# Optimization experiments

Measured on AMD Instinct MI355X. Metric: run time of the kernel, lower is better.

The kernel has to match this reference:

```python
import jax, jax.numpy as jnp
import numpy as np

N_USERS = 100000
N_ITEMS = 50000
N_NODES = N_USERS + N_ITEMS
D = 64
N_INTENTS = 128
N_LAYERS = 2
E = 3200000
E_U = 1600000
E_I = 800000
N_MP = 2


def spmm(idx, vals, x, n):
    # sparse (n,n) COO @ dense (n,d): out[r] = sum_e vals[e] * x[c[e]] where idx=[rows;cols]
    return jax.ops.segment_sum(vals[:, None] * x[idx[1]], idx[0], num_segments=n)


def graph_conv_both(edges, h, n):
    # DGL GraphConv(norm='both', weight=None, bias=None, allow_zero_in_degree=True)
    src, dst = edges[0], edges[1]
    ones = jnp.ones(src.shape[0], h.dtype)
    deg_out = jax.ops.segment_sum(ones, src, num_segments=n)
    deg_in = jax.ops.segment_sum(ones, dst, num_segments=n)
    inv = lambda d: jnp.where(d > 0, jax.lax.rsqrt(jnp.maximum(d, 1e-12)), 0.0)
    hs = h * inv(deg_out)[:, None]
    agg = jax.ops.segment_sum(hs[src], dst, num_segments=n)
    return agg * inv(deg_in)[:, None]


def semantic_attention(z, W1, b1, w2):
    # z: (N, M, D)
    w = jnp.tanh(z @ W1 + b1) @ w2        # (N, M)
    beta = jax.nn.softmax(w.mean(0))       # (M,)
    return jnp.einsum('m,nmd->nd', beta, z)


def dccf(G_indices, G_values, feat_user, feat_item, user_intent, item_intent):
    emb = jnp.concatenate([feat_user, feat_item], axis=0)
    total = emb
    cur = emb
    for _ in range(N_LAYERS):
        gnn = spmm(G_indices, G_values, cur, N_NODES)
        u, it = cur[:N_USERS], cur[N_USERS:]
        u_int = jax.nn.softmax(u @ user_intent, axis=1) @ user_intent.T
        i_int = jax.nn.softmax(it @ item_intent, axis=1) @ item_intent.T
        cur = gnn + jnp.concatenate([u_int, i_int], axis=0) + cur
        total = total + cur
    return total[:N_USERS], total[N_USERS:]


def han(mp_edges, h, n, W1, b1, w2):
    z = jnp.stack([graph_conv_both(mp_edges[m], h, n) for m in range(N_MP)], axis=1)
    return semantic_attention(z, W1, b1, w2)


def setup_inputs() -> dict:
    key = jax.random.key(0)
    ks = jax.random.split(key, 16)
    s = 1.0 / np.sqrt(D)
    return {
        'G_indices': jax.random.randint(ks[0], (2, E), 0, N_NODES),
        'G_values': jax.random.uniform(ks[1], (E,), jnp.float32),
        'feat_user': jax.random.normal(ks[2], (N_USERS, D), jnp.float32) * s,
        'feat_item': jax.random.normal(ks[3], (N_ITEMS, D), jnp.float32) * s,
        'user_intent': jax.random.normal(ks[4], (D, N_INTENTS), jnp.float32) * s,
        'item_intent': jax.random.normal(ks[5], (D, N_INTENTS), jnp.float32) * s,
        'mp_user_edges': jax.random.randint(ks[6], (N_MP, 2, E_U), 0, N_USERS),
        'mp_item_edges': jax.random.randint(ks[7], (N_MP, 2, E_I), 0, N_ITEMS),
        'sem_user_W1': jax.random.normal(ks[8], (D, 128), jnp.float32) * s,
        'sem_user_b1': jnp.zeros((128,), jnp.float32),
        'sem_user_w2': jax.random.normal(ks[9], (128,), jnp.float32) * s,
        'sem_item_W1': jax.random.normal(ks[10], (D, 128), jnp.float32) * s,
        'sem_item_b1': jnp.zeros((128,), jnp.float32),
        'sem_item_w2': jax.random.normal(ks[11], (128,), jnp.float32) * s,
        'user_idx': jax.random.randint(ks[12], (1024,), 0, N_USERS),
        'item_idx': jax.random.randint(ks[13], (1024,), 0, N_ITEMS),
        'neg_item_idx': jax.random.randint(ks[14], (1024,), 0, N_ITEMS),
    }


def reference(G_indices, G_values, feat_user, feat_item, user_intent, item_intent,
              mp_user_edges, mp_item_edges,
              sem_user_W1, sem_user_b1, sem_user_w2,
              sem_item_W1, sem_item_b1, sem_item_w2,
              user_idx, item_idx, neg_item_idx):
    ua, ia = dccf(G_indices, G_values, feat_user, feat_item, user_intent, item_intent)
    h_user = han(mp_user_edges, feat_user, N_USERS, sem_user_W1, sem_user_b1, sem_user_w2)
    h_item = han(mp_item_edges, feat_item, N_ITEMS, sem_item_W1, sem_item_b1, sem_item_w2)
    user_emb = 0.5 * ua + 0.5 * h_user
    item_emb = 0.5 * ia + 0.5 * h_item
    return (user_emb, item_emb)
```

## Files before the change

### kernel.cpp

```cpp
#include <hip/hip_runtime.h>
#include <hip/hip_bf16.h>
#include <math.h>

#define N_USERS 100000
#define N_ITEMS 50000
#define N_NODES 150000
#define DD 64
#define E_G 3200000
#define EU 1600000
#define EI 800000
#define E_HAN 4800000
#define NH 300000
#define NBG 293
#define NBH 586
#define ROWS 32

__device__ __forceinline__ float invdeg(float d){
  return d > 0.f ? rsqrtf(fmaxf(d, 1e-12f)) : 0.f;
}
__device__ __forceinline__ float tanh_fast(float x){
  float cx = fminf(15.f, fmaxf(-15.f, x));
  float t = __expf(2.f*cx);
  return (t - 1.f)/(t + 1.f);
}
__device__ __forceinline__ unsigned short f2b(float x){
  unsigned int b = __float_as_uint(x);
  b += 0x7FFFu + ((b >> 16) & 1u);
  return (unsigned short)(b >> 16);
}
__device__ __forceinline__ float b2f(unsigned short u){
  return __uint_as_float(((unsigned int)u) << 16);
}
__device__ __forceinline__ float b2f_lo(unsigned int u){
  return __uint_as_float(u << 16);
}
__device__ __forceinline__ float b2f_hi(unsigned int u){
  return __uint_as_float(u & 0xFFFF0000u);
}

__global__ void k_init(const float* __restrict__ fu, const float* __restrict__ fi,
                       float* __restrict__ cur, float* __restrict__ total){
  int i = blockIdx.x*256 + threadIdx.x;
  if (i >= N_NODES*DD) return;
  float v = (i < N_USERS*DD) ? fu[i] : fi[i - N_USERS*DD];
  cur[i] = v; total[i] = v;
}

__global__ __launch_bounds__(256) void k_colscan(int* __restrict__ wh, int nb,
                                                 int* __restrict__ colsum){
  __shared__ int s[256];
  int b = blockIdx.x, tid = threadIdx.x;
  int v = wh[tid*nb + b];
  s[tid] = v; __syncthreads();
  for (int o = 1; o < 256; o <<= 1){
    int t = (tid >= o) ? s[tid - o] : 0;
    __syncthreads();
    s[tid] += t;
    __syncthreads();
  }
  wh[tid*nb + b] = s[tid] - v;
  if (tid == 255) colsum[b] = s[255];
}

__global__ __launch_bounds__(256) void k_bscan(const int* __restrict__ colsum, int nb,
                                               int total, int* __restrict__ bB){
  __shared__ int s[256];
  __shared__ int carry;
  int tid = threadIdx.x;
  if (tid == 0) carry = 0;
  __syncthreads();
  for (int base = 0; base < nb; base += 256){
    int i = base + tid;
    int v = (i < nb) ? colsum[i] : 0;
    s[tid] = v; __syncthreads();
    for (int o = 1; o < 256; o <<= 1){
      int t = (tid >= o) ? s[tid - o] : 0;
      __syncthreads();
      s[tid] += t;
      __syncthreads();
    }
    int c = carry;
    if (i < nb) bB[i] = c + s[tid] - v;
    __syncthreads();
    if (tid == 255) carry = c + s[255];
    __syncthreads();
  }
  if (tid == 0) bB[nb] = total;
}

__global__ __launch_bounds__(256) void k_h1_g(const int* __restrict__ gi,
                                              int* __restrict__ wh){
  __shared__ int h[NBG];
  int tid = threadIdx.x;
  for (int b = tid; b < NBG; b += 256) h[b] = 0;
  __syncthreads();
  int e0 = blockIdx.x*(E_G/256);
  for (int i = tid; i < E_G/256; i += 256)
    atomicAdd(&h[gi[e0 + i] >> 9], 1);
  __syncthreads();
  for (int b = tid; b < NBG; b += 256) wh[blockIdx.x*NBG + b] = h[b];
}

__global__ __launch_bounds__(256) void k_h2_g(const int* __restrict__ gi,
        const float* __restrict__ gv, const int* __restrict__ wh,
        const int* __restrict__ bB, uint2* __restrict__ kv){
  __shared__ int lcur[NBG];
  int tid = threadIdx.x, wg = blockIdx.x;
  for (int b = tid; b < NBG; b += 256) lcur[b] = bB[b] + wh[wg*NBG + b];
  __syncthreads();
  int e0 = wg*(E_G/256);
  for (int i = tid; i < E_G/256; i += 256){
    int e = e0 + i;
    int d = gi[e];
    int p = atomicAdd(&lcur[d >> 9], 1);
    uint2 r;
    r.x = ((unsigned)(d & 511) << 18) | (unsigned)gi[E_G + e];
    r.y = __float_as_uint(gv[e]);
    kv[p] = r;
  }
}

__global__ __launch_bounds__(256) void k_p2_g(const int* __restrict__ bB,
        const uint2* __restrict__ kv, int* __restrict__ off,
        unsigned int* __restrict__ packed){
  __shared__ int cnt[512], sc[512], lcur[512];
  int b = blockIdx.x, tid = threadIdx.x;
  int d0 = b << 9;
  int dcnt = min(512, N_NODES - d0);
  int pb = bB[b], pe = bB[b+1];
  for (int i = tid; i < 512; i += 256) cnt[i] = 0;
  __syncthreads();
  for (int p = pb + tid; p < pe; p += 256)
    atomicAdd(&cnt[kv[p].x >> 18], 1);
  __syncthreads();
  sc[tid] = cnt[tid]; sc[tid + 256] = cnt[tid + 256];
  __syncthreads();
  for (int o = 1; o < 512; o <<= 1){
    int a0 = (tid >= o) ? sc[tid - o] : 0;
    int a1 = sc[tid + 256 - o];
    __syncthreads();
    sc[tid] += a0; sc[tid + 256] += a1;
    __syncthreads();
  }
  for (int i = tid; i < 512; i += 256) lcur[i] = pb + sc[i] - cnt[i];
  for (int i = tid; i < dcnt; i += 256) off[d0 + i] = pb + sc[i] - cnt[i];
  if (tid == 0) off[d0 + dcnt] = pe;
  __syncthreads();
  for (int p = pb + tid; p < pe; p += 256){
    uint2 r = kv[p];
    int dl = (int)(r.x >> 18);
    unsigned int s = r.x & 0x3FFFFu;
    float v = __uint_as_float(r.y);
    int q14 = (int)(v*16383.f + 0.5f);
    if (q14 > 16383) q14 = 16383;
    int q = atomicAdd(&lcur[dl], 1);
    packed[q] = (s << 14) | (unsigned int)q14;
  }
}

__global__ __launch_bounds__(256) void k_spmm_gp(const int* __restrict__ off,
        const unsigned int* __restrict__ packed,
        const float* __restrict__ cur, float* __restrict__ gnn){
  int wv = threadIdx.x >> 6, lane = threadIdx.x & 63;
  int node = blockIdx.x*4 + wv;
  if (node >= N_NODES) return;
  int b = off[node], e = off[node+1];
  int c4 = (lane & 15)*4, sl = lane >> 4;
  float ax=0.f, ay=0.f, az=0.f, aw=0.f;
  const float inv14 = 1.f/16383.f;
  for (int k = b; k < e; k += 8){
    int i0 = k + sl, i1 = i0 + 4;
    bool v0 = i0 < e, v1 = i1 < e;
    unsigned int pk0 = v0 ? packed[i0] : 0u;
    unsigned int pk1 = v1 ? packed[i1] : 0u;
    int s0 = (int)(pk0 >> 14), s1 = (int)(pk1 >> 14);
    float w0 = (float)(pk0 & 16383u) * inv14;
    float w1 = (float)(pk1 & 16383u) * inv14;
    const float4 x0 = *(const float4*)&cur[s0*DD + c4];
    const float4 x1 = *(const float4*)&cur[s1*DD + c4];
    ax += w0*x0.x; ay += w0*x0.y; az += w0*x0.z; aw += w0*x0.w;
    ax += w1*x1.x; ay += w1*x1.y; az += w1*x1.z; aw += w1*x1.w;
  }
  ax += __shfl_xor(ax, 16, 64); ay += __shfl_xor(ay, 16, 64);
  az += __shfl_xor(az, 16, 64); aw += __shfl_xor(aw, 16, 64);
  ax += __shfl_xor(ax, 32, 64); ay += __shfl_xor(ay, 32, 64);
  az += __shfl_xor(az, 32, 64); aw += __shfl_xor(aw, 32, 64);
  if (lane < 16) *(float4*)&gnn[node*DD + c4] = make_float4(ax, ay, az, aw);
}

__global__ __launch_bounds__(256) void k_intent2(const float* __restrict__ intent,
        const float* __restrict__ gnn, float* __restrict__ cur, float* __restrict__ total,
        int base, int nrows){
  __shared__ float sB[64*132];
  __shared__ float sU[ROWS*132];
  int tid = threadIdx.x, tx = tid & 15, ty = tid >> 4;

  for (int i = tid; i < 2048; i += 256){
    int r = i >> 5, c = (i & 31) << 2;
    *(float4*)&sB[r*132 + c] = *(const float4*)&intent[r*128 + c];
  }
  {
    int r = tid & 31, q0 = tid >> 5;
    int rr = blockIdx.x*ROWS + r;
    int rowg = base + (rr < nrows ? rr : nrows - 1);
    for (int q = q0; q < 16; q += 8){
      float4 v = *(const float4*)&cur[rowg*DD + 4*q];
      sU[(4*q+0)*36 + r] = v.x;
      sU[(4*q+1)*36 + r] = v.y;
      sU[(4*q+2)*36 + r] = v.z;
      sU[(4*q+3)*36 + r] = v.w;
    }
  }
  __syncthreads();

  float w[2][8];
  #pragma unroll
  for (int i = 0; i < 2; ++i)
    #pragma unroll
    for (int k = 0; k < 8; ++k) w[i][k] = 0.f;
  for (int d = 0; d < 64; ++d){
    float2 a = *(const float2*)&sU[d*36 + 2*ty];
    float4 b0 = *(const float4*)&sB[d*132 + 8*tx];
    float4 b1 = *(const float4*)&sB[d*132 + 8*tx + 4];
    float bb[8] = {b0.x,b0.y,b0.z,b0.w,b1.x,b1.y,b1.z,b1.w};
    #pragma unroll
    for (int k = 0; k < 8; ++k){ w[0][k] += a.x*bb[k]; w[1][k] += a.y*bb[k]; }
  }

  float p[2][8];
  #pragma unroll
  for (int i = 0; i < 2; ++i){
    float mx = w[i][0];
    #pragma unroll
    for (int k = 1; k < 8; ++k) mx = fmaxf(mx, w[i][k]);
    mx = fmaxf(mx, __shfl_xor(mx, 1, 64));
    mx = fmaxf(mx, __shfl_xor(mx, 2, 64));
    mx = fmaxf(mx, __shfl_xor(mx, 4, 64));
    mx = fmaxf(mx, __shfl_xor(mx, 8, 64));
    float s = 0.f;
    #pragma unroll
    for (int k = 0; k < 8; ++k){ p[i][k] = __expf(w[i][k] - mx); s += p[i][k]; }
    s += __shfl_xor(s, 1, 64);
    s += __shfl_xor(s, 2, 64);
    s += __shfl_xor(s, 4, 64);
    s += __shfl_xor(s, 8, 64);
    float inv = 1.f / s;
    #pragma unroll
    for (int k = 0; k < 8; ++k) p[i][k] *= inv;
  }
  __syncthreads();
  #pragma unroll
  for (int i = 0; i < 2; ++i){
    *(float4*)&sU[(2*ty+i)*132 + 8*tx]     = make_float4(p[i][0],p[i][1],p[i][2],p[i][3]);
    *(float4*)&sU[(2*ty+i)*132 + 8*tx + 4] = make_float4(p[i][4],p[i][5],p[i][6],p[i][7]);
  }
  __syncthreads();

  float o[2][4];
  #pragma unroll
  for (int i = 0; i < 2; ++i)
    #pragma unroll
    for (int m = 0; m < 4; ++m) o[i][m] = 0.f;
  for (int q = 0; q < 32; ++q){
    float4 p0 = *(const float4*)&sU[(2*ty+0)*132 + 4*q];
    float4 p1 = *(const float4*)&sU[(2*ty+1)*132 + 4*q];
    #pragma unroll
    for (int m = 0; m < 4; ++m){
      float4 bl = *(const float4*)&sB[(4*tx+m)*132 + 4*q];
      o[0][m] += p0.x*bl.x + p0.y*bl.y + p0.z*bl.z + p0.w*bl.w;
      o[1][m] += p1.x*bl.x + p1.y*bl.y + p1.z*bl.z + p1.w*bl.w;
    }
  }

  #pragma unroll
  for (int i = 0; i < 2; ++i){
    int rr = blockIdx.x*ROWS + 2*ty + i;
    if (rr < nrows){
      int rowg = base + rr;
      float4 g = *(const float4*)&gnn[rowg*DD + 4*tx];
      float4 c = *(const float4*)&cur[rowg*DD + 4*tx];
      float4 t = *(const float4*)&total[rowg*DD + 4*tx];
      float4 cn = make_float4(g.x + o[i][0] + c.x, g.y + o[i][1] + c.y,
                              g.z + o[i][2] + c.z, g.w + o[i][3] + c.w);
      *(float4*)&cur[rowg*DD + 4*tx] = cn;
      *(float4*)&total[rowg*DD + 4*tx] =
          make_float4(t.x + cn.x, t.y + cn.y, t.z + cn.z, t.w + cn.w);
    }
  }
}

__device__ __forceinline__ void han_decode(int t, const int* mp_u, const int* mp_i,
                                           int* gs, int* gd){
  if (t < 2*EU){
    int s = (t < EU) ? 0 : 1;
    int e = t - s*EU;
    const int* sp = mp_u + (long)s*2*EU;
    int nb = s*N_USERS;
    *gs = nb + sp[e]; *gd = nb + sp[EU + e];
  } else {
    int t2 = t - 2*EU;
    int s = (t2 < EI) ? 0 : 1;
    int e = t2 - s*EI;
    const int* sp = mp_i + (long)s*2*EI;
    int nb = 2*N_USERS + s*N_ITEMS;
    *gs = nb + sp[e]; *gd = nb + sp[EI + e];
  }
}

__global__ __launch_bounds__(256) void k_h1_h(const int* __restrict__ mp_u,
        const int* __restrict__ mp_i, int* __restrict__ whD, int* __restrict__ whS){
  __shared__ int hd[NBH], hs[NBH];
  int tid = threadIdx.x;
  for (int b = tid; b < NBH; b += 256){ hd[b] = 0; hs[b] = 0; }
  __syncthreads();
  int t0 = blockIdx.x*(E_HAN/256);
  for (int i = tid; i < E_HAN/256; i += 256){
    int gs, gd;
    han_decode(t0 + i, mp_u, mp_i, &gs, &gd);
    atomicAdd(&hd[gd >> 9], 1);
    atomicAdd(&hs[gs >> 9], 1);
  }
  __syncthreads();
  for (int b = tid; b < NBH; b += 256){
    whD[blockIdx.x*NBH + b] = hd[b];
    whS[blockIdx.x*NBH + b] = hs[b];
  }
}

__global__ __launch_bounds__(256) void k_h2_h(const int* __restrict__ mp_u,
        const int* __restrict__ mp_i, const int* __restrict__ whD,
        const int* __restrict__ whS, const int* __restrict__ bBD,
        const int* __restrict__ bBS, unsigned int* __restrict__ keyD,
        int* __restrict__ keyS){
  __shared__ int lcD[NBH], lcS[NBH];
  int tid = threadIdx.x, wg = blockIdx.x;
  for (int b = tid; b < NBH; b += 256){
    lcD[b] = bBD[b] + whD[wg*NBH + b];
    lcS[b] = bBS[b] + whS[wg*NBH + b];
  }
  __syncthreads();
  int t0 = wg*(E_HAN/256);
  for (int i = tid; i < E_HAN/256; i += 256){
    int gs, gd;
    han_decode(t0 + i, mp_u, mp_i, &gs, &gd);
    int pD = atomicAdd(&lcD[gd >> 9], 1);
    keyD[pD] = ((unsigned)(gd & 511) << 19) | (unsigned)gs;
    int pS = atomicAdd(&lcS[gs >> 9], 1);
    keyS[pS] = gs;
  }
}

__global__ __launch_bounds__(256) void k_p2_h(const int* __restrict__ bB,
        const unsigned int* __restrict__ key, int* __restrict__ off,
        int* __restrict__ ssrc){
  __shared__ int cnt[512], sc[512], lcur[512];
  int b = blockIdx.x, tid = threadIdx.x;
  int d0 = b << 9;
  int dcnt = min(512, NH - d0);
  int pb = bB[b], pe = bB[b+1];
  for (int i = tid; i < 512; i += 256) cnt[i] = 0;
  __syncthreads();
  for (int p = pb + tid; p < pe; p += 256)
    atomicAdd(&cnt[key[p] >> 19], 1);
  __syncthreads();
  sc[tid] = cnt[tid]; sc[tid + 256] = cnt[tid + 256];
  __syncthreads();
  for (int o = 1; o < 512; o <<= 1){
    int a0 = (tid >= o) ? sc[tid - o] : 0;
    int a1 = sc[tid + 256 - o];
    __syncthreads();
    sc[tid] += a0; sc[tid + 256] += a1;
    __syncthreads();
  }
  for (int i = tid; i < 512; i += 256) lcur[i] = pb + sc[i] - cnt[i];
  for (int i = tid; i < dcnt; i += 256) off[d0 + i] = pb + sc[i] - cnt[i];
  if (tid == 0) off[d0 + dcnt] = pe;
  __syncthreads();
  for (int p = pb + tid; p < pe; p += 256){
    unsigned int k = key[p];
    int dl = (int)(k >> 19);
    int q = atomicAdd(&lcur[dl], 1);
    ssrc[q] = (int)(k & 0x7FFFFu);
  }
}

__global__ __launch_bounds__(256) void k_cnt_hs(const int* __restrict__ bB,
        const int* __restrict__ keyS, int* __restrict__ dego){
  __shared__ int cnt[512];
  int b = blockIdx.x, tid = threadIdx.x;
  int d0 = b << 9;
  int dcnt = min(512, NH - d0);
  int pb = bB[b], pe = bB[b+1];
  for (int i = tid; i < 512; i += 256) cnt[i] = 0;
  __syncthreads();
  for (int p = pb + tid; p < pe; p += 256)
    atomicAdd(&cnt[keyS[p] & 511], 1);
  __syncthreads();
  for (int i = tid; i < dcnt; i += 256) dego[d0 + i] = cnt[i];
}

__global__ void k_gtab(const int* __restrict__ degout, const float* __restrict__ fu,
                       const float* __restrict__ fi, unsigned short* __restrict__ gtab){
  int i = blockIdx.x*256 + threadIdx.x;
  if (i >= NH*DD) return;
  int n = i >> 6, d = i & 63;
  float f;
  if (n < 2*N_USERS){
    int local = (n < N_USERS) ? n : n - N_USERS;
    f = fu[local*DD + d];
  } else {
    int m = n - 2*N_USERS;
    int local = (m < N_ITEMS) ? m : m - N_ITEMS;
    f = fi[local*DD + d];
  }
  gtab[i] = f2b(invdeg((float)degout[n]) * f);
}

__global__ __launch_bounds__(256) void k_han_gb(const int* __restrict__ off,
        const int* __restrict__ ssrc, const unsigned short* __restrict__ gtab,
        unsigned short* __restrict__ zb){
  int wv = threadIdx.x >> 6, lane = threadIdx.x & 63;
  int g = blockIdx.x*4 + wv;
  if (g >= NH) return;
  int b = off[g], e = off[g+1];
  int c8 = (lane & 7)*8, sl = lane >> 3;
  float a[8];
  #pragma unroll
  for (int j = 0; j < 8; ++j) a[j] = 0.f;
  for (int k = b; k < e; k += 16){
    int i0 = k + sl, i1 = i0 + 8;
    bool v0 = i0 < e, v1 = i1 < e;
    int s0 = v0 ? ssrc[i0] : 0;
    int s1 = v1 ? ssrc[i1] : 0;
    const uint4 u0 = *(const uint4*)&gtab[s0*DD + c8];
    const uint4 u1 = *(const uint4*)&gtab[s1*DD + c8];
    float m0 = v0 ? 1.f : 0.f, m1 = v1 ? 1.f : 0.f;
    a[0] = fmaf(m0, b2f_lo(u0.x), a[0]); a[1] = fmaf(m0, b2f_hi(u0.x), a[1]);
    a[2] = fmaf(m0, b2f_lo(u0.y), a[2]); a[3] = fmaf(m0, b2f_hi(u0.y), a[3]);
    a[4] = fmaf(m0, b2f_lo(u0.z), a[4]); a[5] = fmaf(m0, b2f_hi(u0.z), a[5]);
    a[6] = fmaf(m0, b2f_lo(u0.w), a[6]); a[7] = fmaf(m0, b2f_hi(u0.w), a[7]);
    a[0] = fmaf(m1, b2f_lo(u1.x), a[0]); a[1] = fmaf(m1, b2f_hi(u1.x), a[1]);
    a[2] = fmaf(m1, b2f_lo(u1.y), a[2]); a[3] = fmaf(m1, b2f_hi(u1.y), a[3]);
    a[4] = fmaf(m1, b2f_lo(u1.z), a[4]); a[5] = fmaf(m1, b2f_hi(u1.z), a[5]);
    a[6] = fmaf(m1, b2f_lo(u1.w), a[6]); a[7] = fmaf(m1, b2f_hi(u1.w), a[7]);
  }
  #pragma unroll
  for (int j = 0; j < 8; ++j){
    a[j] += __shfl_xor(a[j], 8, 64);
    a[j] += __shfl_xor(a[j], 16, 64);
    a[j] += __shfl_xor(a[j], 32, 64);
  }
  if (lane < 8){
    float win = invdeg((float)(e - b));
    uint4 o;
    o.x = (unsigned)f2b(win*a[0]) | ((unsigned)f2b(win*a[1]) << 16);
    o.y = (unsigned)f2b(win*a[2]) | ((unsigned)f2b(win*a[3]) << 16);
    o.z = (unsigned)f2b(win*a[4]) | ((unsigned)f2b(win*a[5]) << 16);
    o.w = (unsigned)f2b(win*a[6]) | ((unsigned)f2b(win*a[7]) << 16);
    *(uint4*)&zb[g*DD + c8] = o;
  }
}

__global__ __launch_bounds__(256) void k_sem2(const float* __restrict__ W1,
        const float* __restrict__ b1, const float* __restrict__ w2,
        const unsigned short* __restrict__ z, int nn, float* __restrict__ wsum){
  __shared__ float sW[64*132];
  __shared__ float sA[64*36];
  __shared__ float sBias[128], sV[128];
  __shared__ float red[2];
  int tid = threadIdx.x, tx = tid & 15, ty = tid >> 4;

  for (int i = tid; i < 2048; i += 256){
    int r = i >> 5, c = (i & 31) << 2;
    *(float4*)&sW[r*132 + c] = *(const float4*)&W1[r*128 + c];
  }
  if (tid < 128){ sBias[tid] = b1[tid]; sV[tid] = w2[tid]; }
  if (tid < 2) red[tid] = 0.f;

  for (int m = 0; m < 2; ++m){
    __syncthreads();
    {
      int r = tid & 31, q0 = tid >> 5;
      int rr = blockIdx.x*ROWS + r;
      int rowg = (rr < nn ? rr : nn - 1) + m*nn;
      for (int q = q0; q < 16; q += 8){
        ushort4 v = *(const ushort4*)&z[(long)rowg*DD + 4*q];
        sA[(4*q+0)*36 + r] = b2f(v.x);
        sA[(4*q+1)*36 + r] = b2f(v.y);
        sA[(4*q+2)*36 + r] = b2f(v.z);
        sA[(4*q+3)*36 + r] = b2f(v.w);
      }
    }
    __syncthreads();

    float w[2][8];
    #pragma unroll
    for (int i = 0; i < 2; ++i)
      #pragma unroll
      for (int k = 0; k < 8; ++k) w[i][k] = sBias[8*tx + k];
    for (int d = 0; d < 64; ++d){
      float2 a = *(const float2*)&sA[d*36 + 2*ty];
      float4 b0 = *(const float4*)&sW[d*132 + 8*tx];
      float4 b4 = *(const float4*)&sW[d*132 + 8*tx + 4];
      float bb[8] = {b0.x,b0.y,b0.z,b0.w,b4.x,b4.y,b4.z,b4.w};
      #pragma unroll
      for (int k = 0; k < 8; ++k){ w[0][k] += a.x*bb[k]; w[1][k] += a.y*bb[k]; }
    }
    float part = 0.f;
    #pragma unroll
    for (int i = 0; i < 2; ++i){
      int rr = blockIdx.x*ROWS + 2*ty + i;
      if (rr < nn){
        #pragma unroll
        for (int k = 0; k < 8; ++k) part += tanh_fast(w[i][k]) * sV[8*tx + k];
      }
    }
    part += __shfl_xor(part, 1, 64);
    part += __shfl_xor(part, 2, 64);
    part += __shfl_xor(part, 4, 64);
    part += __shfl_xor(part, 8, 64);
    part += __shfl_xor(part, 16, 64);
    part += __shfl_xor(part, 32, 64);
    if ((tid & 63) == 0) atomicAdd(&red[m], part);
  }
  __syncthreads();
  if (tid < 2) atomicAdd(&wsum[tid], red[tid]);
}

__global__ void k_beta(const float* __restrict__ wsum, float* __restrict__ beta){
  if (threadIdx.x == 0 && blockIdx.x == 0){
    float u0 = wsum[0] / (float)N_USERS, u1 = wsum[1] / (float)N_USERS;
    float m = fmaxf(u0, u1);
    float e0 = __expf(u0 - m), e1 = __expf(u1 - m);
    beta[0] = e0/(e0+e1); beta[1] = e1/(e0+e1);
    float i0 = wsum[2] / (float)N_ITEMS, i1 = wsum[3] / (float)N_ITEMS;
    m = fmaxf(i0, i1);
    e0 = __expf(i0 - m); e1 = __expf(i1 - m);
    beta[2] = e0/(e0+e1); beta[3] = e1/(e0+e1);
  }
}

__global__ void k_final(const float* __restrict__ total, const unsigned short* __restrict__ zb,
                        const float* __restrict__ beta, float* __restrict__ out){
  int i = blockIdx.x*256 + threadIdx.x;
  if (i >= N_NODES*DD) return;
  float h;
  if (i < N_USERS*DD)
    h = beta[0]*b2f(zb[i]) + beta[1]*b2f(zb[N_USERS*DD + i]);
  else {
    int j = i - N_USERS*DD;
    h = beta[2]*b2f(zb[2*N_USERS*DD + j]) + beta[3]*b2f(zb[(2*N_USERS + N_ITEMS)*DD + j]);
  }
  out[i] = 0.5f*total[i] + 0.5f*h;
}

extern "C" void kernel_launch(void* const* d_in, const int* in_sizes, int n_in,
                              void* d_out, int out_size, void* d_ws, size_t ws_size,
                              hipStream_t stream) {
  const int*   G_idx = (const int*)d_in[0];
  const float* G_val = (const float*)d_in[1];
  const float* fu    = (const float*)d_in[2];
  const float* fi    = (const float*)d_in[3];
  const float* u_int = (const float*)d_in[4];
  const float* i_int = (const float*)d_in[5];
  const int*   mp_u  = (const int*)d_in[6];
  const int*   mp_i  = (const int*)d_in[7];
  const float* uW1   = (const float*)d_in[8];
  const float* ub1   = (const float*)d_in[9];
  const float* uw2   = (const float*)d_in[10];
  const float* iW1   = (const float*)d_in[11];
  const float* ib1   = (const float*)d_in[12];
  const float* iw2   = (const float*)d_in[13];
  float* out = (float*)d_out;

  float* ws = (float*)d_ws;
  float*        total  = ws;
  float*        cur    = ws + 9600000;
  float*        gnn    = ws + 19200000;
  uint2*        kvG    = (uint2*)ws;
  unsigned int* packG  = (unsigned int*)(ws + 28800000);
  int*          offG   = (int*)(ws + 33700000);
  int*          whG    = (int*)(ws + 34930000);
  int*          colG   = (int*)(ws + 35018000);
  int*          bBG    = (int*)(ws + 35019000);
  unsigned int* keyH   = (unsigned int*)(ws + 9600000);
  unsigned short* zb   = (unsigned short*)(ws + 9600000);
  int*          keyS   = (int*)(ws + 19200000);
  unsigned short* gtab = (unsigned short*)(ws + 19200000);
  int*          ssrcH  = (int*)(ws + 28800000);
  int*          degoH  = (int*)(ws + 34000000);
  int*          offH   = (int*)(ws + 34300000);
  int*          whH    = (int*)(ws + 34610000);
  int*          whS    = (int*)(ws + 34770000);
  int*          colH   = (int*)(ws + 35010000);
  int*          bBH    = (int*)(ws + 35012000);
  int*          colS   = (int*)(ws + 35014000);
  int*          bBS    = (int*)(ws + 35016000);
  float*        wsum   = ws + 35030000;
  float*        beta   = ws + 35030004;

  hipMemsetAsync(wsum, 0, 4*sizeof(float), stream);

  k_h1_g<<<256, 256, 0, stream>>>(G_idx, whG);
  k_colscan<<<NBG, 256, 0, stream>>>(whG, NBG, colG);
  k_bscan<<<1, 256, 0, stream>>>(colG, NBG, E_G, bBG);
  k_h2_g<<<256, 256, 0, stream>>>(G_idx, G_val, whG, bBG, kvG);
  k_p2_g<<<NBG, 256, 0, stream>>>(bBG, kvG, offG, packG);

  k_init<<<(N_NODES*DD + 255)/256, 256, 0, stream>>>(fu, fi, cur, total);

  for (int layer = 0; layer < 2; ++layer){
    k_spmm_gp<<<(N_NODES + 3)/4, 256, 0, stream>>>(offG, packG, cur, gnn);
    k_intent2<<<(N_USERS + ROWS-1)/ROWS, 256, 0, stream>>>(u_int, gnn, cur, total, 0, N_USERS);
    k_intent2<<<(N_ITEMS + ROWS-1)/ROWS, 256, 0, stream>>>(i_int, gnn, cur, total, N_USERS, N_ITEMS);
  }

  k_h1_h<<<256, 256, 0, stream>>>(mp_u, mp_i, whH, whS);
  k_colscan<<<NBH, 256, 0, stream>>>(whH, NBH, colH);
  k_bscan<<<1, 256, 0, stream>>>(colH, NBH, E_HAN, bBH);
  k_colscan<<<NBH, 256, 0, stream>>>(whS, NBH, colS);
  k_bscan<<<1, 256, 0, stream>>>(colS, NBH, E_HAN, bBS);
  k_h2_h<<<256, 256, 0, stream>>>(mp_u, mp_i, whH, whS, bBH, bBS, keyH, keyS);
  k_p2_h<<<NBH, 256, 0, stream>>>(bBH, keyH, offH, ssrcH);
  k_cnt_hs<<<NBH, 256, 0, stream>>>(bBS, keyS, degoH);
  k_gtab<<<(NH*DD + 255)/256, 256, 0, stream>>>(degoH, fu, fi, gtab);
  k_han_gb<<<(NH + 3)/4, 256, 0, stream>>>(offH, ssrcH, gtab, zb);

  k_sem2<<<(N_USERS + ROWS-1)/ROWS, 256, 0, stream>>>(uW1, ub1, uw2, zb, N_USERS, wsum);
  k_sem2<<<(N_ITEMS + ROWS-1)/ROWS, 256, 0, stream>>>(iW1, ib1, iw2,
      zb + (long)2*N_USERS*DD, N_ITEMS, wsum + 2);
  k_beta<<<1, 64, 0, stream>>>(wsum, beta);
  k_final<<<(N_NODES*DD + 255)/256, 256, 0, stream>>>(total, zb, beta, out);
}
```

Measured before the change: 1.270 ms.

## Fold HAN source normalization into packed edge weights and unroll SpMM gather

The HAN aggregation previously gathered from a per-metapath, degree-prescaled bf16 table of 300K rows. Now the source out-degree normalization is quantized into 14 bits packed next to the source node index in each edge record, so the gather reads a shared 150K-row bf16 feature table. This halves the table built and gathered and removes the per-element degree lookup, but the per-edge weight quantization adds error. The graph SpMM loop is also unrolled to issue four gathers per iteration for more memory-level parallelism.

```diff
diff --git a/kernel.cpp b/kernel.cpp
--- a/kernel.cpp
+++ b/kernel.cpp
@@ -168,18 +168,26 @@
   int c4 = (lane & 15)*4, sl = lane >> 4;
   float ax=0.f, ay=0.f, az=0.f, aw=0.f;
   const float inv14 = 1.f/16383.f;
-  for (int k = b; k < e; k += 8){
-    int i0 = k + sl, i1 = i0 + 4;
-    bool v0 = i0 < e, v1 = i1 < e;
-    unsigned int pk0 = v0 ? packed[i0] : 0u;
-    unsigned int pk1 = v1 ? packed[i1] : 0u;
-    int s0 = (int)(pk0 >> 14), s1 = (int)(pk1 >> 14);
-    float w0 = (float)(pk0 & 16383u) * inv14;
-    float w1 = (float)(pk1 & 16383u) * inv14;
-    const float4 x0 = *(const float4*)&cur[s0*DD + c4];
-    const float4 x1 = *(const float4*)&cur[s1*DD + c4];
-    ax += w0*x0.x; ay += w0*x0.y; az += w0*x0.z; aw += w0*x0.w;
-    ax += w1*x1.x; ay += w1*x1.y; az += w1*x1.z; aw += w1*x1.w;
+  for (int k = b; k < e; k += 16){
+    unsigned int pk[4];
+    float4 x[4];
+    float w[4];
+    #pragma unroll
+    for (int j = 0; j < 4; ++j){
+      int idx = k + sl + 4*j;
+      pk[j] = (idx < e) ? packed[idx] : 0u;
+    }
+    #pragma unroll
+    for (int j = 0; j < 4; ++j){
+      int s = (int)(pk[j] >> 14);
+      w[j] = (float)(pk[j] & 16383u) * inv14;
+      x[j] = *(const float4*)&cur[s*DD + c4];
+    }
+    #pragma unroll
+    for (int j = 0; j < 4; ++j){
+      ax += w[j]*x[j].x; ay += w[j]*x[j].y;
+      az += w[j]*x[j].z; aw += w[j]*x[j].w;
+    }
   }
   ax += __shfl_xor(ax, 16, 64); ay += __shfl_xor(ay, 16, 64);
   az += __shfl_xor(az, 16, 64); aw += __shfl_xor(aw, 16, 64);
@@ -351,8 +359,8 @@
 }
 
 __global__ __launch_bounds__(256) void k_p2_h(const int* __restrict__ bB,
-        const unsigned int* __restrict__ key, int* __restrict__ off,
-        int* __restrict__ ssrc){
+        const unsigned int* __restrict__ key, const int* __restrict__ dego,
+        int* __restrict__ off, unsigned int* __restrict__ ssrc){
   __shared__ int cnt[512], sc[512], lcur[512];
   int b = blockIdx.x, tid = threadIdx.x;
   int d0 = b << 9;
@@ -379,8 +387,13 @@
   for (int p = pb + tid; p < pe; p += 256){
     unsigned int k = key[p];
     int dl = (int)(k >> 19);
+    int gs = (int)(k & 0x7FFFFu);
+    int fsrc = gs - (gs >= N_USERS ? N_USERS : 0) - (gs >= 250000 ? 50000 : 0);
+    float w = invdeg((float)dego[gs]);
+    int q14 = (int)(w*16383.f + 0.5f);
+    if (q14 > 16383) q14 = 16383;
     int q = atomicAdd(&lcur[dl], 1);
-    ssrc[q] = (int)(k & 0x7FFFFu);
+    ssrc[q] = ((unsigned)fsrc << 14) | (unsigned)q14;
   }
 }
 
@@ -399,50 +412,43 @@
   for (int i = tid; i < dcnt; i += 256) dego[d0 + i] = cnt[i];
 }
 
-__global__ void k_gtab(const int* __restrict__ degout, const float* __restrict__ fu,
-                       const float* __restrict__ fi, unsigned short* __restrict__ gtab){
+__global__ void k_fb(const float* __restrict__ fu, const float* __restrict__ fi,
+                     unsigned short* __restrict__ fb){
   int i = blockIdx.x*256 + threadIdx.x;
-  if (i >= NH*DD) return;
-  int n = i >> 6, d = i & 63;
-  float f;
-  if (n < 2*N_USERS){
-    int local = (n < N_USERS) ? n : n - N_USERS;
-    f = fu[local*DD + d];
-  } else {
-    int m = n - 2*N_USERS;
-    int local = (m < N_ITEMS) ? m : m - N_ITEMS;
-    f = fi[local*DD + d];
-  }
-  gtab[i] = f2b(invdeg((float)degout[n]) * f);
+  if (i >= N_NODES*DD) return;
+  float f = (i < N_USERS*DD) ? fu[i] : fi[i - N_USERS*DD];
+  fb[i] = f2b(f);
 }
 
 __global__ __launch_bounds__(256) void k_han_gb(const int* __restrict__ off,
-        const int* __restrict__ ssrc, const unsigned short* __restrict__ gtab,
+        const unsigned int* __restrict__ ssrc, const unsigned short* __restrict__ fb,
         unsigned short* __restrict__ zb){
   int wv = threadIdx.x >> 6, lane = threadIdx.x & 63;
   int g = blockIdx.x*4 + wv;
   if (g >= NH) return;
   int b = off[g], e = off[g+1];
   int c8 = (lane & 7)*8, sl = lane >> 3;
+  const float inv14 = 1.f/16383.f;
   float a[8];
   #pragma unroll
   for (int j = 0; j < 8; ++j) a[j] = 0.f;
   for (int k = b; k < e; k += 16){
     int i0 = k + sl, i1 = i0 + 8;
-    bool v0 = i0 < e, v1 = i1 < e;
-    int s0 = v0 ? ssrc[i0] : 0;
-    int s1 = v1 ? ssrc[i1] : 0;
-    const uint4 u0 = *(const uint4*)&gtab[s0*DD + c8];
-    const uint4 u1 = *(const uint4*)&gtab[s1*DD + c8];
-    float m0 = v0 ? 1.f : 0.f, m1 = v1 ? 1.f : 0.f;
-    a[0] = fmaf(m0, b2f_lo(u0.x), a[0]); a[1] = fmaf(m0, b2f_hi(u0.x), a[1]);
-    a[2] = fmaf(m0, b2f_lo(u0.y), a[2]); a[3] = fmaf(m0, b2f_hi(u0.y), a[3]);
-    a[4] = fmaf(m0, b2f_lo(u0.z), a[4]); a[5] = fmaf(m0, b2f_hi(u0.z), a[5]);
-    a[6] = fmaf(m0, b2f_lo(u0.w), a[6]); a[7] = fmaf(m0, b2f_hi(u0.w), a[7]);
-    a[0] = fmaf(m1, b2f_lo(u1.x), a[0]); a[1] = fmaf(m1, b2f_hi(u1.x), a[1]);
-    a[2] = fmaf(m1, b2f_lo(u1.y), a[2]); a[3] = fmaf(m1, b2f_hi(u1.y), a[3]);
-    a[4] = fmaf(m1, b2f_lo(u1.z), a[4]); a[5] = fmaf(m1, b2f_hi(u1.z), a[5]);
-    a[6] = fmaf(m1, b2f_lo(u1.w), a[6]); a[7] = fmaf(m1, b2f_hi(u1.w), a[7]);
+    unsigned int pk0 = (i0 < e) ? ssrc[i0] : 0u;
+    unsigned int pk1 = (i1 < e) ? ssrc[i1] : 0u;
+    int s0 = (int)(pk0 >> 14), s1 = (int)(pk1 >> 14);
+    float w0 = (float)(pk0 & 16383u) * inv14;
+    float w1 = (float)(pk1 & 16383u) * inv14;
+    const uint4 u0 = *(const uint4*)&fb[s0*DD + c8];
+    const uint4 u1 = *(const uint4*)&fb[s1*DD + c8];
+    a[0] = fmaf(w0, b2f_lo(u0.x), a[0]); a[1] = fmaf(w0, b2f_hi(u0.x), a[1]);
+    a[2] = fmaf(w0, b2f_lo(u0.y), a[2]); a[3] = fmaf(w0, b2f_hi(u0.y), a[3]);
+    a[4] = fmaf(w0, b2f_lo(u0.z), a[4]); a[5] = fmaf(w0, b2f_hi(u0.z), a[5]);
+    a[6] = fmaf(w0, b2f_lo(u0.w), a[6]); a[7] = fmaf(w0, b2f_hi(u0.w), a[7]);
+    a[0] = fmaf(w1, b2f_lo(u1.x), a[0]); a[1] = fmaf(w1, b2f_hi(u1.x), a[1]);
+    a[2] = fmaf(w1, b2f_lo(u1.y), a[2]); a[3] = fmaf(w1, b2f_hi(u1.y), a[3]);
+    a[4] = fmaf(w1, b2f_lo(u1.z), a[4]); a[5] = fmaf(w1, b2f_hi(u1.z), a[5]);
+    a[6] = fmaf(w1, b2f_lo(u1.w), a[6]); a[7] = fmaf(w1, b2f_hi(u1.w), a[7]);
   }
   #pragma unroll
   for (int j = 0; j < 8; ++j){
@@ -586,8 +592,8 @@
   unsigned int* keyH   = (unsigned int*)(ws + 9600000);
   unsigned short* zb   = (unsigned short*)(ws + 9600000);
   int*          keyS   = (int*)(ws + 19200000);
-  unsigned short* gtab = (unsigned short*)(ws + 19200000);
-  int*          ssrcH  = (int*)(ws + 28800000);
+  unsigned short* fb   = (unsigned short*)(ws + 19200000);
+  unsigned int* ssrcH  = (unsigned int*)(ws + 28800000);
   int*          degoH  = (int*)(ws + 34000000);
   int*          offH   = (int*)(ws + 34300000);
   int*          whH    = (int*)(ws + 34610000);
@@ -621,10 +627,10 @@
   k_colscan<<<NBH, 256, 0, stream>>>(whS, NBH, colS);
   k_bscan<<<1, 256, 0, stream>>>(colS, NBH, E_HAN, bBS);
   k_h2_h<<<256, 256, 0, stream>>>(mp_u, mp_i, whH, whS, bBH, bBS, keyH, keyS);
-  k_p2_h<<<NBH, 256, 0, stream>>>(bBH, keyH, offH, ssrcH);
   k_cnt_hs<<<NBH, 256, 0, stream>>>(bBS, keyS, degoH);
-  k_gtab<<<(NH*DD + 255)/256, 256, 0, stream>>>(degoH, fu, fi, gtab);
-  k_han_gb<<<(NH + 3)/4, 256, 0, stream>>>(offH, ssrcH, gtab, zb);
+  k_fb<<<(N_NODES*DD + 255)/256, 256, 0, stream>>>(fu, fi, fb);
+  k_p2_h<<<NBH, 256, 0, stream>>>(bBH, keyH, degoH, offH, ssrcH);
+  k_han_gb<<<(NH + 3)/4, 256, 0, stream>>>(offH, ssrcH, fb, zb);
 
   k_sem2<<<(N_USERS + ROWS-1)/ROWS, 256, 0, stream>>>(uW1, ub1, uw2, zb, N_USERS, wsum);
   k_sem2<<<(N_ITEMS + ROWS-1)/ROWS, 256, 0, stream>>>(iW1, ib1, iw2,
```

Result: no change. 1.272 ms (+0.2%).
